# Performance work log

Measured on AMD Instinct MI355X. Metric: run time of the kernel, lower is better.

The kernel has to match this reference:

```python
import jax, jax.numpy as jnp
import numpy as np

N = 32768       # batch of states
DQ = 8          # q_ndim (dof_ndim)
A = 4           # action_dim
H = 1024        # hidden_size


def setup_inputs() -> dict:
    key = jax.random.key(0)
    ks = jax.random.split(key, 16)

    def lin(kw, kb, fan_out, fan_in, zero_bias=False):
        s = 1.0 / np.sqrt(fan_in)
        W = jax.random.normal(kw, (fan_out, fan_in), dtype=jnp.float32) * s
        b = jnp.zeros((fan_out,), jnp.float32) if zero_bias else \
            jax.random.normal(kb, (fan_out,), dtype=jnp.float32) * s
        return W, b

    W1, b1 = lin(ks[0], ks[1], H, 2 * DQ)            # h_net layer 1
    W2, b2 = lin(ks[2], ks[3], H, H)                 # h_net layer 2
    Wh, bh = lin(ks[4], ks[5], 1, H)                 # h_net head -> scalar H(z)
    Wf1, bf1 = lin(ks[6], ks[7], H, 2 * DQ + A)      # flex_net layer 1
    Wf2, bf2 = lin(ks[8], ks[9], H, H)               # flex_net layer 2
    Wff, bff = lin(ks[10], ks[11], 2 * DQ, H)        # flex_net head -> 2*q_ndim
    Wp, bp = lin(ks[12], ks[13], A, 2 * DQ)          # control policy (detached)

    return {
        "t": jnp.zeros((), jnp.float32),
        "z": jax.random.normal(ks[14], (N, 2 * DQ), dtype=jnp.float32),
        "W1": W1, "b1": b1, "W2": W2, "b2": b2, "Wh": Wh, "bh": bh,
        "Wf1": Wf1, "bf1": bf1, "Wf2": Wf2, "bf2": bf2, "Wff": Wff, "bff": bff,
        "Wp": Wp, "bp": bp,
    }


def reference(t, z, W1, b1, W2, b2, Wh, bh,
              Wf1, bf1, Wf2, bf2, Wff, bff, Wp, bp):
    # control input, detached as in the torch forward (u = policy(t, z).detach())
    u = jax.lax.stop_gradient(jnp.tanh(z @ Wp.T + bp))  # [N, A]

    # ---- H-net forward, saving tanh' at each activation (the `sps` list) ----
    # angular_dims=() -> CosSin is the identity, so h_net[0](z) = z.
    a1 = z @ W1.T + b1          # [N, H]
    h1 = jnp.tanh(a1)
    s0 = 1.0 - h1 * h1          # d tanh / d a1   (sps[0])
    a2 = h1 @ W2.T + b2         # [N, H]
    h2 = jnp.tanh(a2)
    s1 = 1.0 - h2 * h2          # d tanh / d a2   (sps[1])

    # dH = grad_z sum(h_net(z)), with gradients flowing (create_graph=True)
    def H_sum(zz):
        hh = jnp.tanh(zz @ W1.T + b1)
        hh = jnp.tanh(hh @ W2.T + b2)
        return jnp.sum(hh @ Wh.T + bh)

    dH = jax.grad(H_sum)(z)     # [N, 2*DQ]

    # ---- flex-net with skip term modulated by reversed tanh' maps ----
    zu = jnp.concatenate([z, u], axis=-1)       # [N, 2*DQ + A]
    f1 = zu @ Wf1.T + bf1
    g1 = jnp.tanh(f1) + f1 * s1                 # idx = 1 -> sps[1]
    f2 = g1 @ Wf2.T + bf2
    g2 = jnp.tanh(f2) + f2 * s0                 # idx = 0 -> sps[0]
    out = g2 @ Wff.T + bff                      # [N, 2*DQ]

    # D = jacobian of CosSin = identity per batch row (angular_dims=()), so
    # bmm(out[:,None,:], D).squeeze(1) == out.

    # dz_dt = J @ (out + dH):  J([top; bot]) = [bot; -top]
    s = out + dH
    return jnp.concatenate([s[:, DQ:], -s[:, :DQ]], axis=-1)  # [N, 2*DQ]
```

## Files before the change

kernel.cpp:

```cpp
#include <hip/hip_runtime.h>
#include <hip/hip_bf16.h>

typedef __hip_bfloat16 bf16;
typedef __attribute__((ext_vector_type(8))) short short8;
typedef __attribute__((ext_vector_type(4))) short s16x4;
typedef __attribute__((ext_vector_type(4))) float f32x4;

__device__ __forceinline__ bf16 f2b(float f) { return __float2bfloat16(f); }
__device__ __forceinline__ short bfbits(float f) {
  union { float f; unsigned u; } x; x.f = f;
  unsigned r = x.u + 0x7fff + ((x.u >> 16) & 1);
  return (short)(r >> 16);
}
__device__ __forceinline__ float tanh_fast(float x) {
  float t = __expf(-2.f * fabsf(x));
  float r = (1.f - t) * __builtin_amdgcn_rcpf(1.f + t);
  return copysignf(r, x);
}

#define GLOAD_LDS16(gp, lp) __builtin_amdgcn_global_load_lds( \
    (const __attribute__((address_space(1))) void*)(gp), \
    (__attribute__((address_space(3))) void*)(lp), 16, 0, 0)
#define SBAR() __builtin_amdgcn_s_barrier()
#define WAITV(n) do { asm volatile("s_waitcnt vmcnt(" #n ")" ::: "memory"); \
                      __builtin_amdgcn_sched_barrier(0); } while (0)

__global__ __launch_bounds__(256) void prep(
    const float* __restrict__ W2, const float* __restrict__ Wf2,
    const float* __restrict__ W1, const float* __restrict__ Wff,
    bf16* __restrict__ W2bf, bf16* __restrict__ W2Tbf,
    bf16* __restrict__ Wf2bf, bf16* __restrict__ W1n,
    bf16* __restrict__ Wffn)
{
  __shared__ float T[32][33];
  const int tid = threadIdx.x, bx = blockIdx.x;
  const int tx = bx & 31, ty = bx >> 5;
  const int r = tid >> 3, c4 = (tid & 7) * 4;
  const long ibase = (long)(ty * 32 + r) * 1024 + tx * 32 + c4;

  f32x4 v = *(const f32x4*)(W2 + ibase);
  f32x4 vf = *(const f32x4*)(Wf2 + ibase);
  s16x4 sv, sf;
  #pragma unroll
  for (int j = 0; j < 4; ++j) {
    sv[j] = bfbits(v[j]); sf[j] = bfbits(vf[j]);
    T[r][c4 + j] = v[j];
  }
  *(s16x4*)(W2bf + ibase) = sv;
  *(s16x4*)(Wf2bf + ibase) = sf;
  __syncthreads();
  const int oc = tid >> 3, or4 = (tid & 7) * 4;
  s16x4 st;
  #pragma unroll
  for (int j = 0; j < 4; ++j) st[j] = bfbits(T[or4 + j][oc]);
  *(s16x4*)(W2Tbf + (long)(tx * 32 + oc) * 1024 + ty * 32 + or4) = st;

  if (bx < 32) {
    #pragma unroll
    for (int rep = 0; rep < 2; ++rep) {
      int i = bx * 512 + rep * 256 + tid;
      int rr = i >> 10, cc = i & 1023;
      W1n[i] = f2b(W1[cc * 16 + rr]);
      Wffn[i] = f2b(Wff[i]);
    }
  }
}

__global__ __launch_bounds__(256) void k1(
    const float* __restrict__ z, const float* __restrict__ W1,
    const float* __restrict__ b1, const float* __restrict__ Wp,
    const float* __restrict__ bp, const float* __restrict__ Wf1,
    const float* __restrict__ bf1v,
    bf16* __restrict__ h1, bf16* __restrict__ f1out, long grow0)
{
  __shared__ float zs[32][16];
  __shared__ float us[32][4];
  const int tid = threadIdx.x;
  const long r0 = (long)blockIdx.x * 32;
  for (int i = tid; i < 512; i += 256) {
    int r = i >> 4, c = i & 15;
    zs[r][c] = z[(grow0 + r0 + r) * 16 + c];
  }
  __syncthreads();
  if (tid < 128) {
    int r = tid >> 2, a = tid & 3;
    float acc = bp[a];
    #pragma unroll
    for (int k = 0; k < 16; ++k) acc = fmaf(zs[r][k], Wp[a * 16 + k], acc);
    us[r][a] = tanh_fast(acc);
  }
  __syncthreads();
  #pragma unroll
  for (int jj = 0; jj < 4; ++jj) {
    const int c = tid + jj * 256;
    {
      float w[16];
      #pragma unroll
      for (int k = 0; k < 16; ++k) w[k] = W1[c * 16 + k];
      const float bc = b1[c];
      for (int r = 0; r < 32; ++r) {
        float a = bc;
        #pragma unroll
        for (int k = 0; k < 16; ++k) a = fmaf(zs[r][k], w[k], a);
        h1[(r0 + r) * 1024 + c] = f2b(tanh_fast(a));
      }
    }
    {
      float wf[20];
      #pragma unroll
      for (int k = 0; k < 20; ++k) wf[k] = Wf1[c * 20 + k];
      const float bfc = bf1v[c];
      for (int r = 0; r < 32; ++r) {
        float f = bfc;
        #pragma unroll
        for (int k = 0; k < 16; ++k) f = fmaf(zs[r][k], wf[k], f);
        #pragma unroll
        for (int a = 0; a < 4; ++a) f = fmaf(us[r][a], wf[16 + a], f);
        f1out[(r0 + r) * 1024 + c] = f2b(f);
      }
    }
  }
}

template<int EPI>
__global__ __launch_bounds__(512, 2) void gemm_k(
    const bf16* __restrict__ A, const bf16* __restrict__ Bp,
    const float* __restrict__ bias, const float* __restrict__ Whv,
    const bf16* __restrict__ h1,
    bf16* O1, bf16* __restrict__ O2,
    const bf16* __restrict__ Wn, float* __restrict__ Pp, int ckRows)
{
  __shared__ __align__(16) char smem[131072];
  const int tid = threadIdx.x;
  const int lane = tid & 63, wid = tid >> 6;
  const int wr = wid >> 2, wc = wid & 3;
  const int fr = lane & 15, kg = lane >> 4;
  const long row0 = (long)blockIdx.x * 256;
  const int col0 = blockIdx.y * 256;

  const int sr0 = tid >> 2;
  const int sk0 = ((tid & 3) ^ ((tid >> 3) & 3)) * 8;
  const int swr = (fr >> 1) & 3;

  const bf16* gA0 = A + (row0 + sr0) * 1024 + sk0;
  const bf16* gB0 = Bp + ((long)col0 + sr0) * 1024 + sk0;
  const int rdA = (wr * 128 + fr) * 32 + (kg ^ swr) * 8;
  const int rdB = (wc * 64 + fr) * 32 + (kg ^ swr) * 8;

  f32x4 acc[8][4] = {};

  auto stage = [&](int b, int k0) {
    bf16* as = (bf16*)smem + b * 8192;
    bf16* bs = (bf16*)smem + 32768 + b * 8192;
    GLOAD_LDS16(gA0 + k0, as + tid * 8);
    GLOAD_LDS16(gA0 + 128 * 1024 + k0, as + 4096 + tid * 8);
    GLOAD_LDS16(gB0 + k0, bs + tid * 8);
    GLOAD_LDS16(gB0 + 128 * 1024 + k0, bs + 4096 + tid * 8);
  };

  stage(0, 0); stage(1, 32); stage(2, 64);
  WAITV(8); SBAR();

  #pragma unroll
  for (int kt = 0; kt < 32; ++kt) {
    if (kt + 3 < 32) stage((kt + 3) & 3, (kt + 3) * 32);
    const bf16* as = (const bf16*)smem + (kt & 3) * 8192;
    const bf16* bs = (const bf16*)smem + 32768 + (kt & 3) * 8192;
    short8 af[8], bfr[4];
    #pragma unroll
    for (int m = 0; m < 8; ++m)
      af[m] = *(const short8*)(as + rdA + m * 512);
    #pragma unroll
    for (int n = 0; n < 4; ++n)
      bfr[n] = *(const short8*)(bs + rdB + n * 512);
    __builtin_amdgcn_s_setprio(1);
    #pragma unroll
    for (int m = 0; m < 8; ++m)
      #pragma unroll
      for (int n = 0; n < 4; ++n)
        acc[m][n] = __builtin_amdgcn_mfma_f32_16x16x32_bf16(af[m], bfr[n], acc[m][n], 0, 0, 0);
    __builtin_amdgcn_s_setprio(0);
    if (kt < 29)       WAITV(8);
    else if (kt == 29) WAITV(4);
    else if (kt == 30) WAITV(0);
    if (kt < 31) SBAR();
  }

  if (EPI == 0) {
    #pragma unroll
    for (int m = 0; m < 8; ++m) {
      const long gr0 = row0 + wr * 128 + m * 16 + kg * 4;
      #pragma unroll
      for (int n = 0; n < 4; ++n) {
        const int gc = col0 + wc * 64 + n * 16 + fr;
        const float b2c = bias[gc], whc = Whv[gc];
        f32x4 v = acc[m][n];
        #pragma unroll
        for (int j = 0; j < 4; ++j) {
          const long idx = (gr0 + j) * 1024 + gc;
          float h = tanh_fast(v[j] + b2c);
          float s1v = 1.f - h * h;
          float f = __bfloat162float(((const bf16*)O1)[idx]);
          O2[idx] = f2b(s1v * whc);
          O1[idx] = f2b(tanh_fast(f) + f * s1v);
        }
      }
    }
  } else {
    __syncthreads();
    bf16* Ot = (bf16*)smem;
    f32x4 pacc[2] = {};
    #pragma unroll
    for (int ph = 0; ph < 2; ++ph) {
      if ((wc >> 1) == ph) {
        #pragma unroll
        for (int m = 0; m < 8; ++m) {
          const int rl0 = wr * 128 + m * 16 + kg * 4;
          const long gr0 = row0 + rl0;
          #pragma unroll
          for (int n = 0; n < 4; ++n) {
            const int cl = (wc & 1) * 64 + n * 16 + fr;
            const int gc = col0 + ph * 128 + cl;
            f32x4 v = acc[m][n];
            #pragma unroll
            for (int j = 0; j < 4; ++j) {
              const long idx = (gr0 + j) * 1024 + gc;
              float x = v[j], g;
              if (EPI == 1) {
                float hh = __bfloat162float(h1[idx]);
                g = x * (1.f - hh * hh);
              } else {
                float f = x + bias[gc];
                float hh = __bfloat162float(h1[idx]);
                g = tanh_fast(f) + f * (1.f - hh * hh);
              }
              Ot[(rl0 + j) * 136 + cl] = f2b(g);
            }
          }
        }
      }
      __syncthreads();
      #pragma unroll
      for (int sub = 0; sub < 2; ++sub) {
        const int rl0 = wid * 32 + sub * 16;
        #pragma unroll
        for (int ks = 0; ks < 4; ++ks) {
          short8 afrag = *(const short8*)(Ot + (rl0 + fr) * 136 + ks * 32 + kg * 8);
          short8 bfrag = *(const short8*)(Wn + fr * 1024 + col0 + ph * 128 + ks * 32 + kg * 8);
          pacc[sub] = __builtin_amdgcn_mfma_f32_16x16x32_bf16(afrag, bfrag, pacc[sub], 0, 0, 0);
        }
      }
      if (ph == 0) __syncthreads();
    }
    #pragma unroll
    for (int sub = 0; sub < 2; ++sub) {
      const int rl0 = wid * 32 + sub * 16;
      #pragma unroll
      for (int j = 0; j < 4; ++j)
        Pp[(((long)blockIdx.y) * ckRows + row0 + rl0 + kg * 4 + j) * 16 + fr] = pacc[sub][j];
    }
  }
}

__global__ __launch_bounds__(256) void k7(
    const float* __restrict__ Pp0, const float* __restrict__ Pp1,
    const float* __restrict__ bff, float* __restrict__ out,
    long grow0, int ckRows)
{
  int i = blockIdx.x * 256 + threadIdx.x;
  int r = i >> 4, j = i & 15, jp = (j + 8) & 15;
  float s = bff[jp];
  #pragma unroll
  for (int cb = 0; cb < 4; ++cb) {
    long o = ((long)cb * ckRows + r) * 16 + jp;
    s += Pp0[o] + Pp1[o];
  }
  out[(grow0 + r) * 16 + j] = (j < 8) ? s : -s;
}

extern "C" void kernel_launch(void* const* d_in, const int* in_sizes, int n_in,
                              void* d_out, int out_size, void* d_ws, size_t ws_size,
                              hipStream_t stream) {
  const float* z   = (const float*)d_in[1];
  const float* W1  = (const float*)d_in[2];
  const float* b1  = (const float*)d_in[3];
  const float* W2  = (const float*)d_in[4];
  const float* b2  = (const float*)d_in[5];
  const float* Wh  = (const float*)d_in[6];
  const float* Wf1 = (const float*)d_in[8];
  const float* bf1 = (const float*)d_in[9];
  const float* Wf2 = (const float*)d_in[10];
  const float* bf2 = (const float*)d_in[11];
  const float* Wff = (const float*)d_in[12];
  const float* bff = (const float*)d_in[13];
  const float* Wp  = (const float*)d_in[14];
  const float* bp  = (const float*)d_in[15];
  float* out = (float*)d_out;
  const int N = in_sizes[1] / 16;

  char* p = (char*)d_ws;
  auto alloc = [&](size_t bytes) {
    char* q = p; p += (bytes + 255) & ~(size_t)255; return q;
  };
  bf16* W2bf  = (bf16*)alloc(1024 * 1024 * 2);
  bf16* W2Tbf = (bf16*)alloc(1024 * 1024 * 2);
  bf16* Wf2bf = (bf16*)alloc(1024 * 1024 * 2);
  bf16* W1n   = (bf16*)alloc(16 * 1024 * 2);
  bf16* Wffn  = (bf16*)alloc(16 * 1024 * 2);
  size_t wbytes = (size_t)(p - (char*)d_ws);

  int CK = N;
  while (CK > 256 && wbytes + (size_t)CK * 6656 > ws_size) CK >>= 1;
  bf16* actA = (bf16*)alloc((size_t)CK * 2048);
  bf16* actB = (bf16*)alloc((size_t)CK * 2048);
  bf16* actD = (bf16*)alloc((size_t)CK * 2048);
  float* Pp0 = (float*)alloc((size_t)CK * 4 * 16 * 4);
  float* Pp1 = (float*)alloc((size_t)CK * 4 * 16 * 4);

  prep<<<1024, 256, 0, stream>>>(W2, Wf2, W1, Wff, W2bf, W2Tbf, Wf2bf, W1n, Wffn);

  const dim3 ggrid(CK / 256, 4);
  for (long r0 = 0; r0 < N; r0 += CK) {
    k1<<<CK / 32, 256, 0, stream>>>(z, W1, b1, Wp, bp, Wf1, bf1, actA, actD, r0);
    gemm_k<0><<<ggrid, 512, 0, stream>>>(
        actA, W2bf, b2, Wh, nullptr, actD, actB, nullptr, nullptr, CK);
    gemm_k<1><<<ggrid, 512, 0, stream>>>(
        actB, W2Tbf, nullptr, nullptr, actA, nullptr, nullptr, W1n, Pp0, CK);
    gemm_k<2><<<ggrid, 512, 0, stream>>>(
        actD, Wf2bf, bf2, nullptr, actA, nullptr, nullptr, Wffn, Pp1, CK);
    k7<<<CK / 16, 256, 0, stream>>>(Pp0, Pp1, bff, out, r0, CK);
  }
}
```

Measured before the change: 346.1 us.

## Fuse backward-H and flex-net layer-2 GEMMs into one dual-accumulator kernel

Replaces the two separate 1024x1024 GEMM launches (H-net backward through W2^T and flex-net layer 2) with a single kernel. Each block stages tiles of both A operands and both weight matrices and keeps two accumulator sets, so the shared h1 tile is read once. Both small head projections are written into one partial buffer with 8 column blocks. The tile shrinks from 256x256 with 512 threads to 128x128 with 256 threads, using a simpler double-buffered pipeline. This cuts launches and h1 traffic but doubles register pressure and weakens the per-operand reuse of the larger tile.

```diff
diff --git a/kernel.cpp b/kernel.cpp
--- a/kernel.cpp
+++ b/kernel.cpp
@@ -122,13 +122,10 @@
   }
 }
 
-template<int EPI>
-__global__ __launch_bounds__(512, 2) void gemm_k(
+__global__ __launch_bounds__(512, 2) void gemm0(
     const bf16* __restrict__ A, const bf16* __restrict__ Bp,
     const float* __restrict__ bias, const float* __restrict__ Whv,
-    const bf16* __restrict__ h1,
-    bf16* O1, bf16* __restrict__ O2,
-    const bf16* __restrict__ Wn, float* __restrict__ Pp, int ckRows)
+    bf16* O1, bf16* __restrict__ O2)
 {
   __shared__ __align__(16) char smem[131072];
   const int tid = threadIdx.x;
@@ -186,95 +183,174 @@
     if (kt < 31) SBAR();
   }
 
-  if (EPI == 0) {
-    #pragma unroll
-    for (int m = 0; m < 8; ++m) {
-      const long gr0 = row0 + wr * 128 + m * 16 + kg * 4;
+  #pragma unroll
+  for (int m = 0; m < 8; ++m) {
+    const long gr0 = row0 + wr * 128 + m * 16 + kg * 4;
+    #pragma unroll
+    for (int n = 0; n < 4; ++n) {
+      const int gc = col0 + wc * 64 + n * 16 + fr;
+      const float b2c = bias[gc], whc = Whv[gc];
+      f32x4 v = acc[m][n];
+      #pragma unroll
+      for (int j = 0; j < 4; ++j) {
+        const long idx = (gr0 + j) * 1024 + gc;
+        float h = tanh_fast(v[j] + b2c);
+        float s1v = 1.f - h * h;
+        float f = __bfloat162float(((const bf16*)O1)[idx]);
+        O2[idx] = f2b(s1v * whc);
+        O1[idx] = f2b(tanh_fast(f) + f * s1v);
+      }
+    }
+  }
+}
+
+__global__ __launch_bounds__(256, 2) void gemm12(
+    const bf16* __restrict__ Ab, const bf16* __restrict__ Af,
+    const bf16* __restrict__ Bw, const bf16* __restrict__ Bf,
+    const float* __restrict__ bf2v, const bf16* __restrict__ h1,
+    const bf16* __restrict__ W1n, const bf16* __restrict__ Wffn,
+    float* __restrict__ Pp, int ckRows)
+{
+  __shared__ __align__(16) char smem[65536];
+  const int tid = threadIdx.x;
+  const int lane = tid & 63, wid = tid >> 6;
+  const int wr = wid >> 1, wc = wid & 1;
+  const int fr = lane & 15, kg = lane >> 4;
+  const long row0 = (long)blockIdx.x * 128;
+  const int col0 = blockIdx.y * 128;
+
+  const int sr0 = tid >> 2;
+  const int sk0 = ((tid & 3) ^ ((tid >> 3) & 3)) * 8;
+  const int swr = (fr >> 1) & 3;
+
+  const bf16* gAb = Ab + (row0 + sr0) * 1024 + sk0;
+  const bf16* gAf = Af + (row0 + sr0) * 1024 + sk0;
+  const bf16* gBw = Bw + ((long)col0 + sr0) * 1024 + sk0;
+  const bf16* gBf = Bf + ((long)col0 + sr0) * 1024 + sk0;
+  const int rdA = (wr * 64 + fr) * 32 + (kg ^ swr) * 8;
+  const int rdB = (wc * 64 + fr) * 32 + (kg ^ swr) * 8;
+
+  f32x4 accB[4][4] = {}, accF[4][4] = {};
+
+  auto stage = [&](int b, int k0) {
+    bf16* s = (bf16*)smem + b * 16384;
+    GLOAD_LDS16(gAb + k0, s + tid * 8);
+    GLOAD_LDS16(gAb + 64 * 1024 + k0, s + 2048 + tid * 8);
+    GLOAD_LDS16(gAf + k0, s + 4096 + tid * 8);
+    GLOAD_LDS16(gAf + 64 * 1024 + k0, s + 6144 + tid * 8);
+    GLOAD_LDS16(gBw + k0, s + 8192 + tid * 8);
+    GLOAD_LDS16(gBw + 64 * 1024 + k0, s + 10240 + tid * 8);
+    GLOAD_LDS16(gBf + k0, s + 12288 + tid * 8);
+    GLOAD_LDS16(gBf + 64 * 1024 + k0, s + 14336 + tid * 8);
+  };
+
+  stage(0, 0);
+  __syncthreads();
+
+  #pragma unroll 2
+  for (int kt = 0; kt < 32; ++kt) {
+    const int cur = kt & 1;
+    if (kt < 31) stage(cur ^ 1, (kt + 1) * 32);
+    const bf16* s = (const bf16*)smem + cur * 16384;
+    short8 afB[4], afF[4], bfW[4], bfFr[4];
+    #pragma unroll
+    for (int m = 0; m < 4; ++m) {
+      afB[m] = *(const short8*)(s + rdA + m * 512);
+      afF[m] = *(const short8*)(s + 4096 + rdA + m * 512);
+    }
+    #pragma unroll
+    for (int n = 0; n < 4; ++n) {
+      bfW[n]  = *(const short8*)(s + 8192 + rdB + n * 512);
+      bfFr[n] = *(const short8*)(s + 12288 + rdB + n * 512);
+    }
+    __builtin_amdgcn_s_setprio(1);
+    #pragma unroll
+    for (int m = 0; m < 4; ++m)
       #pragma unroll
       for (int n = 0; n < 4; ++n) {
-        const int gc = col0 + wc * 64 + n * 16 + fr;
-        const float b2c = bias[gc], whc = Whv[gc];
-        f32x4 v = acc[m][n];
-        #pragma unroll
-        for (int j = 0; j < 4; ++j) {
-          const long idx = (gr0 + j) * 1024 + gc;
-          float h = tanh_fast(v[j] + b2c);
-          float s1v = 1.f - h * h;
-          float f = __bfloat162float(((const bf16*)O1)[idx]);
-          O2[idx] = f2b(s1v * whc);
-          O1[idx] = f2b(tanh_fast(f) + f * s1v);
-        }
-      }
-    }
-  } else {
+        accB[m][n] = __builtin_amdgcn_mfma_f32_16x16x32_bf16(afB[m], bfW[n], accB[m][n], 0, 0, 0);
+        accF[m][n] = __builtin_amdgcn_mfma_f32_16x16x32_bf16(afF[m], bfFr[n], accF[m][n], 0, 0, 0);
+      }
+    __builtin_amdgcn_s_setprio(0);
     __syncthreads();
-    bf16* Ot = (bf16*)smem;
-    f32x4 pacc[2] = {};
-    #pragma unroll
-    for (int ph = 0; ph < 2; ++ph) {
-      if ((wc >> 1) == ph) {
-        #pragma unroll
-        for (int m = 0; m < 8; ++m) {
-          const int rl0 = wr * 128 + m * 16 + kg * 4;
-          const long gr0 = row0 + rl0;
-          #pragma unroll
-          for (int n = 0; n < 4; ++n) {
-            const int cl = (wc & 1) * 64 + n * 16 + fr;
-            const int gc = col0 + ph * 128 + cl;
-            f32x4 v = acc[m][n];
-            #pragma unroll
-            for (int j = 0; j < 4; ++j) {
-              const long idx = (gr0 + j) * 1024 + gc;
-              float x = v[j], g;
-              if (EPI == 1) {
-                float hh = __bfloat162float(h1[idx]);
-                g = x * (1.f - hh * hh);
-              } else {
-                float f = x + bias[gc];
-                float hh = __bfloat162float(h1[idx]);
-                g = tanh_fast(f) + f * (1.f - hh * hh);
-              }
-              Ot[(rl0 + j) * 136 + cl] = f2b(g);
-            }
-          }
-        }
-      }
-      __syncthreads();
-      #pragma unroll
-      for (int sub = 0; sub < 2; ++sub) {
-        const int rl0 = wid * 32 + sub * 16;
-        #pragma unroll
-        for (int ks = 0; ks < 4; ++ks) {
-          short8 afrag = *(const short8*)(Ot + (rl0 + fr) * 136 + ks * 32 + kg * 8);
-          short8 bfrag = *(const short8*)(Wn + fr * 1024 + col0 + ph * 128 + ks * 32 + kg * 8);
-          pacc[sub] = __builtin_amdgcn_mfma_f32_16x16x32_bf16(afrag, bfrag, pacc[sub], 0, 0, 0);
-        }
-      }
-      if (ph == 0) __syncthreads();
-    }
-    #pragma unroll
-    for (int sub = 0; sub < 2; ++sub) {
-      const int rl0 = wid * 32 + sub * 16;
-      #pragma unroll
-      for (int j = 0; j < 4; ++j)
-        Pp[(((long)blockIdx.y) * ckRows + row0 + rl0 + kg * 4 + j) * 16 + fr] = pacc[sub][j];
-    }
+  }
+
+  bf16* Ot = (bf16*)smem;
+  f32x4 pacc[2] = {};
+  #pragma unroll
+  for (int m = 0; m < 4; ++m) {
+    const int rl0 = wr * 64 + m * 16 + kg * 4;
+    const long gr0 = row0 + rl0;
+    #pragma unroll
+    for (int n = 0; n < 4; ++n) {
+      const int cl = wc * 64 + n * 16 + fr;
+      const int gc = col0 + cl;
+      f32x4 v = accB[m][n];
+      #pragma unroll
+      for (int j = 0; j < 4; ++j) {
+        const long idx = (gr0 + j) * 1024 + gc;
+        float hh = __bfloat162float(h1[idx]);
+        Ot[(rl0 + j) * 136 + cl] = f2b(v[j] * (1.f - hh * hh));
+      }
+    }
+  }
+  __syncthreads();
+  #pragma unroll
+  for (int sub = 0; sub < 2; ++sub) {
+    const int rl0 = wid * 32 + sub * 16;
+    #pragma unroll
+    for (int ks = 0; ks < 4; ++ks) {
+      short8 afrag = *(const short8*)(Ot + (rl0 + fr) * 136 + ks * 32 + kg * 8);
+      short8 bfrag = *(const short8*)(W1n + fr * 1024 + col0 + ks * 32 + kg * 8);
+      pacc[sub] = __builtin_amdgcn_mfma_f32_16x16x32_bf16(afrag, bfrag, pacc[sub], 0, 0, 0);
+    }
+  }
+  __syncthreads();
+  #pragma unroll
+  for (int m = 0; m < 4; ++m) {
+    const int rl0 = wr * 64 + m * 16 + kg * 4;
+    const long gr0 = row0 + rl0;
+    #pragma unroll
+    for (int n = 0; n < 4; ++n) {
+      const int cl = wc * 64 + n * 16 + fr;
+      const int gc = col0 + cl;
+      const float bfc = bf2v[gc];
+      f32x4 v = accF[m][n];
+      #pragma unroll
+      for (int j = 0; j < 4; ++j) {
+        const long idx = (gr0 + j) * 1024 + gc;
+        float hh = __bfloat162float(h1[idx]);
+        float f = v[j] + bfc;
+        Ot[(rl0 + j) * 136 + cl] = f2b(tanh_fast(f) + f * (1.f - hh * hh));
+      }
+    }
+  }
+  __syncthreads();
+  #pragma unroll
+  for (int sub = 0; sub < 2; ++sub) {
+    const int rl0 = wid * 32 + sub * 16;
+    #pragma unroll
+    for (int ks = 0; ks < 4; ++ks) {
+      short8 afrag = *(const short8*)(Ot + (rl0 + fr) * 136 + ks * 32 + kg * 8);
+      short8 bfrag = *(const short8*)(Wffn + fr * 1024 + col0 + ks * 32 + kg * 8);
+      pacc[sub] = __builtin_amdgcn_mfma_f32_16x16x32_bf16(afrag, bfrag, pacc[sub], 0, 0, 0);
+    }
+    #pragma unroll
+    for (int j = 0; j < 4; ++j)
+      Pp[(((long)blockIdx.y) * ckRows + row0 + rl0 + kg * 4 + j) * 16 + fr] = pacc[sub][j];
   }
 }
 
 __global__ __launch_bounds__(256) void k7(
-    const float* __restrict__ Pp0, const float* __restrict__ Pp1,
-    const float* __restrict__ bff, float* __restrict__ out,
-    long grow0, int ckRows)
+    const float* __restrict__ Pp, const float* __restrict__ bff,
+    float* __restrict__ out, long grow0, int ckRows)
 {
   int i = blockIdx.x * 256 + threadIdx.x;
   int r = i >> 4, j = i & 15, jp = (j + 8) & 15;
   float s = bff[jp];
   #pragma unroll
-  for (int cb = 0; cb < 4; ++cb) {
-    long o = ((long)cb * ckRows + r) * 16 + jp;
-    s += Pp0[o] + Pp1[o];
-  }
+  for (int cb = 0; cb < 8; ++cb)
+    s += Pp[((long)cb * ckRows + r) * 16 + jp];
   out[(grow0 + r) * 16 + j] = (j < 8) ? s : -s;
 }
 
@@ -314,20 +390,16 @@
   bf16* actA = (bf16*)alloc((size_t)CK * 2048);
   bf16* actB = (bf16*)alloc((size_t)CK * 2048);
   bf16* actD = (bf16*)alloc((size_t)CK * 2048);
-  float* Pp0 = (float*)alloc((size_t)CK * 4 * 16 * 4);
-  float* Pp1 = (float*)alloc((size_t)CK * 4 * 16 * 4);
+  float* Pp  = (float*)alloc((size_t)CK * 8 * 16 * 4);
 
   prep<<<1024, 256, 0, stream>>>(W2, Wf2, W1, Wff, W2bf, W2Tbf, Wf2bf, W1n, Wffn);
 
-  const dim3 ggrid(CK / 256, 4);
   for (long r0 = 0; r0 < N; r0 += CK) {
     k1<<<CK / 32, 256, 0, stream>>>(z, W1, b1, Wp, bp, Wf1, bf1, actA, actD, r0);
-    gemm_k<0><<<ggrid, 512, 0, stream>>>(
-        actA, W2bf, b2, Wh, nullptr, actD, actB, nullptr, nullptr, CK);
-    gemm_k<1><<<ggrid, 512, 0, stream>>>(
-        actB, W2Tbf, nullptr, nullptr, actA, nullptr, nullptr, W1n, Pp0, CK);
-    gemm_k<2><<<ggrid, 512, 0, stream>>>(
-        actD, Wf2bf, bf2, nullptr, actA, nullptr, nullptr, Wffn, Pp1, CK);
-    k7<<<CK / 16, 256, 0, stream>>>(Pp0, Pp1, bff, out, r0, CK);
-  }
-}
+    gemm0<<<dim3(CK / 256, 4), 512, 0, stream>>>(
+        actA, W2bf, b2, Wh, actD, actB);
+    gemm12<<<dim3(CK / 128, 8), 256, 0, stream>>>(
+        actB, actD, W2Tbf, Wf2bf, bf2, actA, W1n, Wffn, Pp, CK);
+    k7<<<CK / 16, 256, 0, stream>>>(Pp, bff, out, r0, CK);
+  }
+}
```

Result: slower. 377.2 us (+9.0%).

## Switch GEMM mainloop to double-buffered 64-wide K tiles with syncthreads

Applied to the files above, without the earlier changes.

Replaces the 4-stage, 32-wide K pipeline with a 2-stage double buffer of 64-wide K tiles. The LDS staging layout and swizzle change to match, and the hand-placed vmcnt waits with raw barriers give way to __syncthreads per iteration. The aim is to halve the barrier count and loop overhead per K. The cost is shallower prefetch, and __syncthreads now waits on the just-issued next-stage loads before the next compute, which risks exposing global load latency.

```diff
diff --git a/kernel.cpp b/kernel.cpp
--- a/kernel.cpp
+++ b/kernel.cpp
@@ -21,9 +21,6 @@
 #define GLOAD_LDS16(gp, lp) __builtin_amdgcn_global_load_lds( \
     (const __attribute__((address_space(1))) void*)(gp), \
     (__attribute__((address_space(3))) void*)(lp), 16, 0, 0)
-#define SBAR() __builtin_amdgcn_s_barrier()
-#define WAITV(n) do { asm volatile("s_waitcnt vmcnt(" #n ")" ::: "memory"); \
-                      __builtin_amdgcn_sched_barrier(0); } while (0)
 
 __global__ __launch_bounds__(256) void prep(
     const float* __restrict__ W2, const float* __restrict__ Wf2,
@@ -138,52 +135,56 @@
   const long row0 = (long)blockIdx.x * 256;
   const int col0 = blockIdx.y * 256;
 
-  const int sr0 = tid >> 2;
-  const int sk0 = ((tid & 3) ^ ((tid >> 3) & 3)) * 8;
+  const int sr0 = tid >> 3;
+  const int sk0 = ((tid >> 2) & 1) * 32 +
+                  (((tid & 3) ^ ((tid >> 4) & 3))) * 8;
   const int swr = (fr >> 1) & 3;
 
   const bf16* gA0 = A + (row0 + sr0) * 1024 + sk0;
   const bf16* gB0 = Bp + ((long)col0 + sr0) * 1024 + sk0;
-  const int rdA = (wr * 128 + fr) * 32 + (kg ^ swr) * 8;
-  const int rdB = (wc * 64 + fr) * 32 + (kg ^ swr) * 8;
+  const int rdA = (wr * 128 + fr) * 64 + (kg ^ swr) * 8;
+  const int rdB = (wc * 64 + fr) * 64 + (kg ^ swr) * 8;
 
   f32x4 acc[8][4] = {};
 
   auto stage = [&](int b, int k0) {
-    bf16* as = (bf16*)smem + b * 8192;
-    bf16* bs = (bf16*)smem + 32768 + b * 8192;
-    GLOAD_LDS16(gA0 + k0, as + tid * 8);
-    GLOAD_LDS16(gA0 + 128 * 1024 + k0, as + 4096 + tid * 8);
-    GLOAD_LDS16(gB0 + k0, bs + tid * 8);
-    GLOAD_LDS16(gB0 + 128 * 1024 + k0, bs + 4096 + tid * 8);
+    bf16* as = (bf16*)smem + b * 16384;
+    bf16* bs = (bf16*)smem + 32768 + b * 16384;
+    #pragma unroll
+    for (int gi = 0; gi < 4; ++gi)
+      GLOAD_LDS16(gA0 + gi * 65536 + k0, as + gi * 4096 + tid * 8);
+    #pragma unroll
+    for (int gi = 0; gi < 4; ++gi)
+      GLOAD_LDS16(gB0 + gi * 65536 + k0, bs + gi * 4096 + tid * 8);
   };
 
-  stage(0, 0); stage(1, 32); stage(2, 64);
-  WAITV(8); SBAR();
-
-  #pragma unroll
-  for (int kt = 0; kt < 32; ++kt) {
-    if (kt + 3 < 32) stage((kt + 3) & 3, (kt + 3) * 32);
-    const bf16* as = (const bf16*)smem + (kt & 3) * 8192;
-    const bf16* bs = (const bf16*)smem + 32768 + (kt & 3) * 8192;
-    short8 af[8], bfr[4];
-    #pragma unroll
-    for (int m = 0; m < 8; ++m)
-      af[m] = *(const short8*)(as + rdA + m * 512);
-    #pragma unroll
-    for (int n = 0; n < 4; ++n)
-      bfr[n] = *(const short8*)(bs + rdB + n * 512);
-    __builtin_amdgcn_s_setprio(1);
-    #pragma unroll
-    for (int m = 0; m < 8; ++m)
+  stage(0, 0);
+  __syncthreads();
+
+  #pragma unroll 2
+  for (int kt = 0; kt < 16; ++kt) {
+    const int cur = kt & 1;
+    if (kt < 15) stage(cur ^ 1, (kt + 1) * 64);
+    const bf16* as = (const bf16*)smem + cur * 16384;
+    const bf16* bs = (const bf16*)smem + 32768 + cur * 16384;
+    #pragma unroll
+    for (int kc = 0; kc < 2; ++kc) {
+      short8 af[8], bfr[4];
+      #pragma unroll
+      for (int m = 0; m < 8; ++m)
+        af[m] = *(const short8*)(as + rdA + m * 1024 + kc * 32);
       #pragma unroll
       for (int n = 0; n < 4; ++n)
-        acc[m][n] = __builtin_amdgcn_mfma_f32_16x16x32_bf16(af[m], bfr[n], acc[m][n], 0, 0, 0);
-    __builtin_amdgcn_s_setprio(0);
-    if (kt < 29)       WAITV(8);
-    else if (kt == 29) WAITV(4);
-    else if (kt == 30) WAITV(0);
-    if (kt < 31) SBAR();
+        bfr[n] = *(const short8*)(bs + rdB + n * 1024 + kc * 32);
+      __builtin_amdgcn_s_setprio(1);
+      #pragma unroll
+      for (int m = 0; m < 8; ++m)
+        #pragma unroll
+        for (int n = 0; n < 4; ++n)
+          acc[m][n] = __builtin_amdgcn_mfma_f32_16x16x32_bf16(af[m], bfr[n], acc[m][n], 0, 0, 0);
+      __builtin_amdgcn_s_setprio(0);
+    }
+    __syncthreads();
   }
 
   if (EPI == 0) {
@@ -207,7 +208,6 @@
       }
     }
   } else {
-    __syncthreads();
     bf16* Ot = (bf16*)smem;
     f32x4 pacc[2] = {};
     #pragma unroll
```

After: 339.2 us (median of 4 runs). 1.02x faster.
